# Kernel optimization log

Hardware: AMD Instinct MI355X
Metric: run time of the kernel (lower is better)

The kernel has to match this reference:

```python
import jax, jax.numpy as jnp
from jax import lax
import numpy as np

N_TOOLS = 50
DIM = 512
N_TOKENS = 8192
PARAM_DIM = 256


def setup_inputs() -> dict:
    key = jax.random.key(0)
    ks = jax.random.split(key, 8)
    s = 1.0 / np.sqrt(DIM)
    x = jax.random.normal(ks[0], (N_TOKENS, DIM), dtype=jnp.float32)
    router_w = jax.random.uniform(ks[1], (N_TOOLS, DIM), jnp.float32, -s, s)
    router_b = jax.random.uniform(ks[2], (N_TOOLS,), jnp.float32, -s, s)
    expert_w = jax.random.uniform(ks[3], (N_TOOLS, DIM, DIM), jnp.float32, -s, s)
    expert_b = jax.random.uniform(ks[4], (N_TOOLS, DIM), jnp.float32, -s, s)
    param_w = jax.random.uniform(ks[5], (PARAM_DIM, DIM), jnp.float32, -s, s)
    param_b = jax.random.uniform(ks[6], (PARAM_DIM,), jnp.float32, -s, s)
    return {"x": x, "router_w": router_w, "router_b": router_b,
            "expert_w": expert_w, "expert_b": expert_b,
            "param_w": param_w, "param_b": param_b}


def _moe_adapt(x, tool_idx, expert_w, expert_b):
    # Top-1 dispatch: for each expert i, y_i = x @ W_i.T + b_i, written only
    # where tool_idx == i. Scan over the fixed 50 experts (mirrors the torch
    # masked per-expert Linear loop) with masked select instead of scatter.
    def step(acc, wb):
        i, W, b = wb
        y = x @ W.T + b  # [N, dim]
        mask = (tool_idx == i)[:, None]
        return jnp.where(mask, y, acc), None

    init = jnp.zeros_like(x)
    acc, _ = lax.scan(step, init, (jnp.arange(N_TOOLS), expert_w, expert_b))
    return acc


def reference(x, router_w, router_b, expert_w, expert_b, param_w, param_b):
    tool_logits = x @ router_w.T + router_b            # [N, 50]
    tool_probs = jax.nn.softmax(tool_logits, axis=-1)   # [N, 50]
    tool_idx = jnp.argmax(tool_probs, axis=-1)          # [N] int
    adapted = _moe_adapt(x, tool_idx, expert_w, expert_b)  # [N, dim]
    params = x @ param_w.T + param_b                    # [N, 256]
    return (tool_idx, tool_probs, adapted, params)
```

## Files before the change

### kernel.cpp

```cpp
#include <hip/hip_runtime.h>
#include <hip/hip_bf16.h>
#include <math.h>

#define N_TOKENS 8192
#define DIM      512
#define N_TOOLS  50
#define PARAM_DIM 256
#define N_ROWBLK (N_TOKENS / 64)
#define MAX_BATCHES 192
#define LDSS 72

typedef float  f32x4 __attribute__((ext_vector_type(4)));
typedef short  s16x8 __attribute__((ext_vector_type(8)));
typedef short  s16x4 __attribute__((ext_vector_type(4)));

#define WS_IDX     0
#define WS_HIST    8192
#define WS_PHIST   14592
#define WS_OFFSETS 20992
#define WS_COUNTS  21056
#define WS_ORDER   21120
#define WS_BE      29312
#define WS_BM0     29504
#define WS_NB      29696

__device__ inline float bf2f(short s) {
    return __uint_as_float(((unsigned)(unsigned short)s) << 16);
}

__device__ inline s16x4 pk4(float a, float b, float c, float d) {
    __hip_bfloat162 p0 = __float22bfloat162_rn(make_float2(a, b));
    __hip_bfloat162 p1 = __float22bfloat162_rn(make_float2(c, d));
    union { __hip_bfloat162 h; short2 s; } u0, u1;
    u0.h = p0; u1.h = p1;
    s16x4 r; r[0] = u0.s.x; r[1] = u0.s.y; r[2] = u1.s.x; r[3] = u1.s.y;
    return r;
}

__global__ __launch_bounds__(256) void head_mfma(const float* __restrict__ x,
                                                 const float* __restrict__ pw,
                                                 const float* __restrict__ pb,
                                                 const float* __restrict__ rw,
                                                 const float* __restrict__ rb,
                                                 float* __restrict__ out_params,
                                                 float* __restrict__ probs,
                                                 float* __restrict__ out_idx,
                                                 int* __restrict__ idx_i,
                                                 int* __restrict__ hist) {
    int r0 = blockIdx.y * 64;
    bool isl = (blockIdx.x == 4);
    int c0 = isl ? 0 : blockIdx.x * 64;

    __shared__ short As[64 * LDSS];
    __shared__ short Bs[64 * LDSS];
    __shared__ short Al[64 * LDSS];
    __shared__ short Bl[64 * LDSS];
    __shared__ int rowcol[64];

    int tid = threadIdx.x;
    int wv = tid >> 6;
    int lane = tid & 63;
    int fm = lane & 15;
    int q = lane >> 4;

    const float* Bsrc = isl ? rw : pw;

    f32x4 acc[4] = {{0.f, 0.f, 0.f, 0.f}, {0.f, 0.f, 0.f, 0.f},
                    {0.f, 0.f, 0.f, 0.f}, {0.f, 0.f, 0.f, 0.f}};

    for (int k0 = 0; k0 < DIM; k0 += 64) {
#pragma unroll
        for (int i = 0; i < 4; ++i) {
            int u = i * 256 + tid;
            int r = u >> 4, g = u & 15;
            float4 v = *(const float4*)&x[(size_t)(r0 + r) * DIM + k0 + g * 4];
            s16x4 h = pk4(v.x, v.y, v.z, v.w);
            *(s16x4*)&As[r * LDSS + g * 4] = h;
            if (isl) {
                s16x4 l = pk4(v.x - bf2f(h[0]), v.y - bf2f(h[1]),
                              v.z - bf2f(h[2]), v.w - bf2f(h[3]));
                *(s16x4*)&Al[r * LDSS + g * 4] = l;
            }
        }
#pragma unroll
        for (int i = 0; i < 4; ++i) {
            int u = i * 256 + tid;
            int c = u >> 4, g = u & 15;
            float4 v = {0.f, 0.f, 0.f, 0.f};
            if (!isl || c < N_TOOLS)
                v = *(const float4*)&Bsrc[(size_t)(c0 + c) * DIM + k0 + g * 4];
            s16x4 h = pk4(v.x, v.y, v.z, v.w);
            *(s16x4*)&Bs[c * LDSS + g * 4] = h;
            if (isl) {
                s16x4 l = pk4(v.x - bf2f(h[0]), v.y - bf2f(h[1]),
                              v.z - bf2f(h[2]), v.w - bf2f(h[3]));
                *(s16x4*)&Bl[c * LDSS + g * 4] = l;
            }
        }
        __syncthreads();

#pragma unroll
        for (int kk = 0; kk < 64; kk += 32) {
            int ao = (wv * 16 + fm) * LDSS + kk + q * 8;
            s16x8 a = *(const s16x8*)&As[ao];
            if (!isl) {
#pragma unroll
                for (int n = 0; n < 4; ++n) {
                    s16x8 b = *(const s16x8*)&Bs[(n * 16 + fm) * LDSS + kk + q * 8];
                    acc[n] = __builtin_amdgcn_mfma_f32_16x16x32_bf16(a, b, acc[n], 0, 0, 0);
                }
            } else {
                s16x8 al = *(const s16x8*)&Al[ao];
#pragma unroll
                for (int n = 0; n < 4; ++n) {
                    int bo = (n * 16 + fm) * LDSS + kk + q * 8;
                    s16x8 b  = *(const s16x8*)&Bs[bo];
                    s16x8 bl = *(const s16x8*)&Bl[bo];
                    acc[n] = __builtin_amdgcn_mfma_f32_16x16x32_bf16(a,  b,  acc[n], 0, 0, 0);
                    acc[n] = __builtin_amdgcn_mfma_f32_16x16x32_bf16(a,  bl, acc[n], 0, 0, 0);
                    acc[n] = __builtin_amdgcn_mfma_f32_16x16x32_bf16(al, b,  acc[n], 0, 0, 0);
                }
            }
        }
        __syncthreads();
    }

    if (!isl) {
        float bias[4];
#pragma unroll
        for (int n = 0; n < 4; ++n) bias[n] = pb[c0 + n * 16 + fm];
#pragma unroll
        for (int r = 0; r < 4; ++r) {
            int row = r0 + wv * 16 + q * 4 + r;
            float* op = out_params + (size_t)row * PARAM_DIM + c0;
#pragma unroll
            for (int n = 0; n < 4; ++n) op[n * 16 + fm] = acc[n][r] + bias[n];
        }
    } else {
        float rbv[4];
#pragma unroll
        for (int n = 0; n < 4; ++n) {
            int c = n * 16 + fm;
            rbv[n] = (c < N_TOOLS) ? rb[c] : 0.f;
        }
#pragma unroll
        for (int rr = 0; rr < 4; ++rr) {
            int row_l = wv * 16 + q * 4 + rr;
            int row = r0 + row_l;
            float v[4];
            float vmax = -INFINITY; int vcol = N_TOOLS;
#pragma unroll
            for (int n = 0; n < 4; ++n) {
                int c = n * 16 + fm;
                v[n] = acc[n][rr] + rbv[n];
                if (c < N_TOOLS && v[n] > vmax) { vmax = v[n]; vcol = c; }
            }
#pragma unroll
            for (int s = 1; s < 16; s <<= 1) {
                float om = __shfl_xor(vmax, s, 64);
                int   oc = __shfl_xor(vcol, s, 64);
                if (om > vmax || (om == vmax && oc < vcol)) { vmax = om; vcol = oc; }
            }
            float e[4]; float esum = 0.f;
#pragma unroll
            for (int n = 0; n < 4; ++n) {
                int c = n * 16 + fm;
                e[n] = (c < N_TOOLS) ? expf(v[n] - vmax) : 0.f;
                esum += e[n];
            }
#pragma unroll
            for (int s = 1; s < 16; s <<= 1) esum += __shfl_xor(esum, s, 64);
            float inv = 1.f / esum;
#pragma unroll
            for (int n = 0; n < 4; ++n) {
                int c = n * 16 + fm;
                if (c < N_TOOLS) probs[(size_t)row * N_TOOLS + c] = e[n] * inv;
            }
            if (fm == 0) {
                out_idx[row] = (float)vcol;
                idx_i[row] = vcol;
                rowcol[row_l] = vcol;
            }
        }
        __syncthreads();
        if (wv == 0) {
            int myc = rowcol[lane];
            int cnt = 0;
            for (int e2 = 0; e2 < N_TOOLS; ++e2) {
                unsigned long long m = __ballot(myc == e2);
                if (lane == e2) cnt = __popcll(m);
            }
            if (lane < N_TOOLS) hist[blockIdx.y * N_TOOLS + lane] = cnt;
        }
    }
}

__global__ void scan_kernel(const int* __restrict__ hist,
                            int* __restrict__ offsets,
                            int* __restrict__ counts,
                            int* __restrict__ phist,
                            int* __restrict__ batch_e,
                            int* __restrict__ batch_m0,
                            int* __restrict__ nb_out) {
    int lane = threadIdx.x;
    int acc_c = 0;
    if (lane < N_TOOLS) {
#pragma unroll 4
        for (int b = 0; b < N_ROWBLK; ++b) {
            int t = hist[b * N_TOOLS + lane];
            phist[b * N_TOOLS + lane] = acc_c;
            acc_c += t;
        }
    }
    int c = (lane < N_TOOLS) ? acc_c : 0;
    int pre = c;
#pragma unroll
    for (int s = 1; s < 64; s <<= 1) {
        int v = __shfl_up(pre, s, 64);
        if (lane >= s) pre += v;
    }
    int excl = pre - c;
    if (lane < N_TOOLS) { offsets[lane] = excl; counts[lane] = c; }

    int nb_i = (lane < N_TOOLS) ? (c + 63) >> 6 : 0;
    int pre2 = nb_i;
#pragma unroll
    for (int s = 1; s < 64; s <<= 1) {
        int v = __shfl_up(pre2, s, 64);
        if (lane >= s) pre2 += v;
    }
    int bstart = pre2 - nb_i;
    for (int b = 0; b < nb_i; ++b) {
        batch_e[bstart + b] = lane;
        batch_m0[bstart + b] = b * 64;
    }
    if (lane == 63) nb_out[0] = pre2;
}

__global__ void reorder_kernel(const int* __restrict__ idx_i,
                               const int* __restrict__ offsets,
                               const int* __restrict__ phist,
                               int* __restrict__ order) {
    int b = blockIdx.x;
    int lane = threadIdx.x;
    int t = b * 64 + lane;
    int e = idx_i[t];
    unsigned long long lt = (1ull << lane) - 1ull;
    int rank = 0;
    for (int ex = 0; ex < N_TOOLS; ++ex) {
        unsigned long long m = __ballot(e == ex);
        if (e == ex) rank = __popcll(m & lt);
    }
    order[offsets[e] + phist[b * N_TOOLS + e] + rank] = t;
}

__global__ __launch_bounds__(256) void adapted_mfma(const float* __restrict__ x,
                                                    const float* __restrict__ ew,
                                                    const float* __restrict__ eb,
                                                    const int* __restrict__ order,
                                                    const int* __restrict__ batch_e,
                                                    const int* __restrict__ batch_m0,
                                                    const int* __restrict__ nb_ptr,
                                                    const int* __restrict__ offsets,
                                                    const int* __restrict__ counts,
                                                    float* __restrict__ out) {
    int b = blockIdx.y;
    if (b >= nb_ptr[0]) return;
    int e = batch_e[b];
    int m0 = batch_m0[b];
    int c0 = blockIdx.x * 64;
    int start = offsets[e] + m0;
    int len = counts[e] - m0;
    if (len > 64) len = 64;

    __shared__ short As[64 * LDSS];
    __shared__ short Bs[64 * LDSS];
    __shared__ int toks[64];

    int tid = threadIdx.x;
    if (tid < 64) toks[tid] = (tid < len) ? order[start + tid] : -1;
    __syncthreads();

    int wv = tid >> 6;
    int lane = tid & 63;
    int fm = lane & 15;
    int q = lane >> 4;

    const float* We = ew + (size_t)e * DIM * DIM;

    f32x4 acc[4] = {{0.f, 0.f, 0.f, 0.f}, {0.f, 0.f, 0.f, 0.f},
                    {0.f, 0.f, 0.f, 0.f}, {0.f, 0.f, 0.f, 0.f}};

    for (int k0 = 0; k0 < DIM; k0 += 64) {
#pragma unroll
        for (int i = 0; i < 4; ++i) {
            int u = i * 256 + tid;
            int r = u >> 4, g = u & 15;
            int tok = toks[r];
            float4 v = {0.f, 0.f, 0.f, 0.f};
            if (tok >= 0) v = *(const float4*)&x[(size_t)tok * DIM + k0 + g * 4];
            *(s16x4*)&As[r * LDSS + g * 4] = pk4(v.x, v.y, v.z, v.w);
        }
#pragma unroll
        for (int i = 0; i < 4; ++i) {
            int u = i * 256 + tid;
            int c = u >> 4, g = u & 15;
            float4 v = *(const float4*)&We[(size_t)(c0 + c) * DIM + k0 + g * 4];
            *(s16x4*)&Bs[c * LDSS + g * 4] = pk4(v.x, v.y, v.z, v.w);
        }
        __syncthreads();

#pragma unroll
        for (int kk = 0; kk < 64; kk += 32) {
            s16x8 a = *(const s16x8*)&As[(wv * 16 + fm) * LDSS + kk + q * 8];
#pragma unroll
            for (int n = 0; n < 4; ++n) {
                s16x8 bf = *(const s16x8*)&Bs[(n * 16 + fm) * LDSS + kk + q * 8];
                acc[n] = __builtin_amdgcn_mfma_f32_16x16x32_bf16(a, bf, acc[n], 0, 0, 0);
            }
        }
        __syncthreads();
    }

    float bias[4];
#pragma unroll
    for (int n = 0; n < 4; ++n) bias[n] = eb[(size_t)e * DIM + c0 + n * 16 + fm];

#pragma unroll
    for (int r = 0; r < 4; ++r) {
        int row = wv * 16 + q * 4 + r;
        int tok = toks[row];
        if (tok < 0) continue;
        float* op = out + (size_t)tok * DIM + c0;
#pragma unroll
        for (int n = 0; n < 4; ++n) op[n * 16 + fm] = acc[n][r] + bias[n];
    }
}

extern "C" void kernel_launch(void* const* d_in, const int* in_sizes, int n_in,
                              void* d_out, int out_size, void* d_ws, size_t ws_size,
                              hipStream_t stream) {
    const float* x        = (const float*)d_in[0];
    const float* router_w = (const float*)d_in[1];
    const float* router_b = (const float*)d_in[2];
    const float* expert_w = (const float*)d_in[3];
    const float* expert_b = (const float*)d_in[4];
    const float* param_w  = (const float*)d_in[5];
    const float* param_b  = (const float*)d_in[6];

    float* out = (float*)d_out;
    float* out_idx     = out;
    float* out_probs   = out + N_TOKENS;
    float* out_adapted = out + N_TOKENS + N_TOKENS * N_TOOLS;
    float* out_params  = out_adapted + (size_t)N_TOKENS * DIM;

    int* ws = (int*)d_ws;
    int* ws_idx     = ws + WS_IDX;
    int* ws_hist    = ws + WS_HIST;
    int* ws_phist   = ws + WS_PHIST;
    int* ws_offsets = ws + WS_OFFSETS;
    int* ws_counts  = ws + WS_COUNTS;
    int* ws_order   = ws + WS_ORDER;
    int* ws_be      = ws + WS_BE;
    int* ws_bm0     = ws + WS_BM0;
    int* ws_nb      = ws + WS_NB;

    head_mfma<<<dim3(5, N_ROWBLK), 256, 0, stream>>>(x, param_w, param_b,
                                                     router_w, router_b,
                                                     out_params, out_probs,
                                                     out_idx, ws_idx, ws_hist);

    scan_kernel<<<1, 64, 0, stream>>>(ws_hist, ws_offsets, ws_counts, ws_phist,
                                      ws_be, ws_bm0, ws_nb);

    reorder_kernel<<<N_ROWBLK, 64, 0, stream>>>(ws_idx, ws_offsets, ws_phist, ws_order);

    adapted_mfma<<<dim3(8, MAX_BATCHES), 256, 0, stream>>>(x, expert_w, expert_b,
                                                           ws_order, ws_be, ws_bm0, ws_nb,
                                                           ws_offsets, ws_counts, out_adapted);
}
```

Baseline: 176.7 us.

## Pre-convert x to bf16 hi/lo, register-prefetch tiles, parallelize histogram scan

Adds a kernel that converts x once into bf16 high and low-residual arrays in workspace, so the head and expert GEMMs load half-width data and no longer repeat the conversion per tile. Both GEMM kernels now prefetch the next K-tile into registers while the current tile is computed, overlapping global loads with MFMA work. The single-wave serial per-block scan is split into a per-expert parallel scan over 50 blocks plus a small offsets kernel. In exchange it adds two kernel launches and extra global traffic to write and reread the converted x.

Result: faster. 155.8 us (-11.8%).

```diff
diff --git a/kernel.cpp b/kernel.cpp
--- a/kernel.cpp
+++ b/kernel.cpp
@@ -23,6 +23,8 @@
 #define WS_BE      29312
 #define WS_BM0     29504
 #define WS_NB      29696
+#define WS_XH      32768
+#define WS_XL      2130944
 
 __device__ inline float bf2f(short s) {
     return __uint_as_float(((unsigned)(unsigned short)s) << 16);
@@ -37,7 +39,20 @@
     return r;
 }
 
-__global__ __launch_bounds__(256) void head_mfma(const float* __restrict__ x,
+__global__ __launch_bounds__(256) void cvt_x_kernel(const float* __restrict__ x,
+                                                    short* __restrict__ xh,
+                                                    short* __restrict__ xl) {
+    size_t i = (size_t)(blockIdx.x * 256 + threadIdx.x) * 4;
+    float4 v = *(const float4*)&x[i];
+    s16x4 h = pk4(v.x, v.y, v.z, v.w);
+    s16x4 l = pk4(v.x - bf2f(h[0]), v.y - bf2f(h[1]),
+                  v.z - bf2f(h[2]), v.w - bf2f(h[3]));
+    *(s16x4*)&xh[i] = h;
+    *(s16x4*)&xl[i] = l;
+}
+
+__global__ __launch_bounds__(256) void head_mfma(const short* __restrict__ xh,
+                                                 const short* __restrict__ xl,
                                                  const float* __restrict__ pw,
                                                  const float* __restrict__ pb,
                                                  const float* __restrict__ rw,
@@ -65,39 +80,71 @@
 
     const float* Bsrc = isl ? rw : pw;
 
+    int ar0 = tid >> 3, ag = tid & 7;
+    int ar1 = ar0 + 32;
+    const short* aptr0 = xh + (size_t)(r0 + ar0) * DIM + ag * 8;
+    const short* aptr1 = xh + (size_t)(r0 + ar1) * DIM + ag * 8;
+    const short* alptr0 = xl + (size_t)(r0 + ar0) * DIM + ag * 8;
+    const short* alptr1 = xl + (size_t)(r0 + ar1) * DIM + ag * 8;
+    int bc[4], bg[4];
+    const float* bptr[4];
+#pragma unroll
+    for (int i = 0; i < 4; ++i) {
+        int u = i * 256 + tid;
+        bc[i] = u >> 4; bg[i] = u & 15;
+        bptr[i] = Bsrc + (size_t)(c0 + bc[i]) * DIM + bg[i] * 4;
+    }
+
     f32x4 acc[4] = {{0.f, 0.f, 0.f, 0.f}, {0.f, 0.f, 0.f, 0.f},
                     {0.f, 0.f, 0.f, 0.f}, {0.f, 0.f, 0.f, 0.f}};
 
+    s16x8 apre0, apre1, alpre0, alpre1;
+    float4 bpre[4];
+    apre0 = *(const s16x8*)aptr0;
+    apre1 = *(const s16x8*)aptr1;
+    if (isl) { alpre0 = *(const s16x8*)alptr0; alpre1 = *(const s16x8*)alptr1; }
+#pragma unroll
+    for (int i = 0; i < 4; ++i) {
+        float4 v = {0.f, 0.f, 0.f, 0.f};
+        if (!isl || bc[i] < N_TOOLS) v = *(const float4*)bptr[i];
+        bpre[i] = v;
+    }
+
     for (int k0 = 0; k0 < DIM; k0 += 64) {
+        *(s16x8*)&As[ar0 * LDSS + ag * 8] = apre0;
+        *(s16x8*)&As[ar1 * LDSS + ag * 8] = apre1;
+        if (isl) {
+            *(s16x8*)&Al[ar0 * LDSS + ag * 8] = alpre0;
+            *(s16x8*)&Al[ar1 * LDSS + ag * 8] = alpre1;
+        }
 #pragma unroll
         for (int i = 0; i < 4; ++i) {
-            int u = i * 256 + tid;
-            int r = u >> 4, g = u & 15;
-            float4 v = *(const float4*)&x[(size_t)(r0 + r) * DIM + k0 + g * 4];
+            float4 v = bpre[i];
             s16x4 h = pk4(v.x, v.y, v.z, v.w);
-            *(s16x4*)&As[r * LDSS + g * 4] = h;
+            *(s16x4*)&Bs[bc[i] * LDSS + bg[i] * 4] = h;
             if (isl) {
                 s16x4 l = pk4(v.x - bf2f(h[0]), v.y - bf2f(h[1]),
                               v.z - bf2f(h[2]), v.w - bf2f(h[3]));
-                *(s16x4*)&Al[r * LDSS + g * 4] = l;
-            }
-        }
-#pragma unroll
-        for (int i = 0; i < 4; ++i) {
-            int u = i * 256 + tid;
-            int c = u >> 4, g = u & 15;
-            float4 v = {0.f, 0.f, 0.f, 0.f};
-            if (!isl || c < N_TOOLS)
-                v = *(const float4*)&Bsrc[(size_t)(c0 + c) * DIM + k0 + g * 4];
-            s16x4 h = pk4(v.x, v.y, v.z, v.w);
-            *(s16x4*)&Bs[c * LDSS + g * 4] = h;
+                *(s16x4*)&Bl[bc[i] * LDSS + bg[i] * 4] = l;
+            }
+        }
+        __syncthreads();
+
+        int kn = k0 + 64;
+        if (kn < DIM) {
+            apre0 = *(const s16x8*)(aptr0 + kn);
+            apre1 = *(const s16x8*)(aptr1 + kn);
             if (isl) {
-                s16x4 l = pk4(v.x - bf2f(h[0]), v.y - bf2f(h[1]),
-                              v.z - bf2f(h[2]), v.w - bf2f(h[3]));
-                *(s16x4*)&Bl[c * LDSS + g * 4] = l;
-            }
-        }
-        __syncthreads();
+                alpre0 = *(const s16x8*)(alptr0 + kn);
+                alpre1 = *(const s16x8*)(alptr1 + kn);
+            }
+#pragma unroll
+            for (int i = 0; i < 4; ++i) {
+                float4 v = {0.f, 0.f, 0.f, 0.f};
+                if (!isl || bc[i] < N_TOOLS) v = *(const float4*)(bptr[i] + kn);
+                bpre[i] = v;
+            }
+        }
 
 #pragma unroll
         for (int kk = 0; kk < 64; kk += 32) {
@@ -195,32 +242,46 @@
     }
 }
 
-__global__ void scan_kernel(const int* __restrict__ hist,
-                            int* __restrict__ offsets,
-                            int* __restrict__ counts,
-                            int* __restrict__ phist,
-                            int* __restrict__ batch_e,
-                            int* __restrict__ batch_m0,
-                            int* __restrict__ nb_out) {
+__global__ void scan1_kernel(const int* __restrict__ hist,
+                             int* __restrict__ phist,
+                             int* __restrict__ counts) {
+    int e = blockIdx.x;
+    int l = threadIdx.x;
+    int v0 = hist[l * N_TOOLS + e];
+    int v1 = hist[(64 + l) * N_TOOLS + e];
+    int s0 = v0;
+#pragma unroll
+    for (int s = 1; s < 64; s <<= 1) {
+        int t = __shfl_up(s0, s, 64);
+        if (l >= s) s0 += t;
+    }
+    int tot0 = __shfl(s0, 63, 64);
+    int s1 = v1;
+#pragma unroll
+    for (int s = 1; s < 64; s <<= 1) {
+        int t = __shfl_up(s1, s, 64);
+        if (l >= s) s1 += t;
+    }
+    s1 += tot0;
+    phist[l * N_TOOLS + e] = s0 - v0;
+    phist[(64 + l) * N_TOOLS + e] = s1 - v1;
+    if (l == 63) counts[e] = s1;
+}
+
+__global__ void scan2_kernel(const int* __restrict__ counts,
+                             int* __restrict__ offsets,
+                             int* __restrict__ batch_e,
+                             int* __restrict__ batch_m0,
+                             int* __restrict__ nb_out) {
     int lane = threadIdx.x;
-    int acc_c = 0;
-    if (lane < N_TOOLS) {
-#pragma unroll 4
-        for (int b = 0; b < N_ROWBLK; ++b) {
-            int t = hist[b * N_TOOLS + lane];
-            phist[b * N_TOOLS + lane] = acc_c;
-            acc_c += t;
-        }
-    }
-    int c = (lane < N_TOOLS) ? acc_c : 0;
+    int c = (lane < N_TOOLS) ? counts[lane] : 0;
     int pre = c;
 #pragma unroll
     for (int s = 1; s < 64; s <<= 1) {
         int v = __shfl_up(pre, s, 64);
         if (lane >= s) pre += v;
     }
-    int excl = pre - c;
-    if (lane < N_TOOLS) { offsets[lane] = excl; counts[lane] = c; }
+    if (lane < N_TOOLS) offsets[lane] = pre - c;
 
     int nb_i = (lane < N_TOOLS) ? (c + 63) >> 6 : 0;
     int pre2 = nb_i;
@@ -254,7 +315,7 @@
     order[offsets[e] + phist[b * N_TOOLS + e] + rank] = t;
 }
 
-__global__ __launch_bounds__(256) void adapted_mfma(const float* __restrict__ x,
+__global__ __launch_bounds__(256) void adapted_mfma(const short* __restrict__ xh,
                                                     const float* __restrict__ ew,
                                                     const float* __restrict__ eb,
                                                     const int* __restrict__ order,
@@ -288,27 +349,47 @@
 
     const float* We = ew + (size_t)e * DIM * DIM;
 
+    int ar0 = tid >> 3, ag = tid & 7;
+    int ar1 = ar0 + 32;
+    int tok0 = toks[ar0], tok1 = toks[ar1];
+    const short* aptr0 = (tok0 >= 0) ? xh + (size_t)tok0 * DIM + ag * 8 : nullptr;
+    const short* aptr1 = (tok1 >= 0) ? xh + (size_t)tok1 * DIM + ag * 8 : nullptr;
+    int bc[4], bg[4];
+    const float* bptr[4];
+#pragma unroll
+    for (int i = 0; i < 4; ++i) {
+        int u = i * 256 + tid;
+        bc[i] = u >> 4; bg[i] = u & 15;
+        bptr[i] = We + (size_t)(c0 + bc[i]) * DIM + bg[i] * 4;
+    }
+
     f32x4 acc[4] = {{0.f, 0.f, 0.f, 0.f}, {0.f, 0.f, 0.f, 0.f},
                     {0.f, 0.f, 0.f, 0.f}, {0.f, 0.f, 0.f, 0.f}};
 
+    const s16x8 z8 = {0, 0, 0, 0, 0, 0, 0, 0};
+    s16x8 apre0 = aptr0 ? *(const s16x8*)aptr0 : z8;
+    s16x8 apre1 = aptr1 ? *(const s16x8*)aptr1 : z8;
+    float4 bpre[4];
+#pragma unroll
+    for (int i = 0; i < 4; ++i) bpre[i] = *(const float4*)bptr[i];
+
     for (int k0 = 0; k0 < DIM; k0 += 64) {
+        *(s16x8*)&As[ar0 * LDSS + ag * 8] = apre0;
+        *(s16x8*)&As[ar1 * LDSS + ag * 8] = apre1;
 #pragma unroll
         for (int i = 0; i < 4; ++i) {
-            int u = i * 256 + tid;
-            int r = u >> 4, g = u & 15;
-            int tok = toks[r];
-            float4 v = {0.f, 0.f, 0.f, 0.f};
-            if (tok >= 0) v = *(const float4*)&x[(size_t)tok * DIM + k0 + g * 4];
-            *(s16x4*)&As[r * LDSS + g * 4] = pk4(v.x, v.y, v.z, v.w);
-        }
-#pragma unroll
-        for (int i = 0; i < 4; ++i) {
-            int u = i * 256 + tid;
-            int c = u >> 4, g = u & 15;
-            float4 v = *(const float4*)&We[(size_t)(c0 + c) * DIM + k0 + g * 4];
-            *(s16x4*)&Bs[c * LDSS + g * 4] = pk4(v.x, v.y, v.z, v.w);
+            float4 v = bpre[i];
+            *(s16x4*)&Bs[bc[i] * LDSS + bg[i] * 4] = pk4(v.x, v.y, v.z, v.w);
         }
         __syncthreads();
+
+        int kn = k0 + 64;
+        if (kn < DIM) {
+            apre0 = aptr0 ? *(const s16x8*)(aptr0 + kn) : z8;
+            apre1 = aptr1 ? *(const s16x8*)(aptr1 + kn) : z8;
+#pragma unroll
+            for (int i = 0; i < 4; ++i) bpre[i] = *(const float4*)(bptr[i] + kn);
+        }
 
 #pragma unroll
         for (int kk = 0; kk < 64; kk += 32) {
@@ -364,18 +445,23 @@
     int* ws_be      = ws + WS_BE;
     int* ws_bm0     = ws + WS_BM0;
     int* ws_nb      = ws + WS_NB;
-
-    head_mfma<<<dim3(5, N_ROWBLK), 256, 0, stream>>>(x, param_w, param_b,
+    short* ws_xh    = (short*)(ws + WS_XH);
+    short* ws_xl    = (short*)(ws + WS_XL);
+
+    cvt_x_kernel<<<N_TOKENS * DIM / 4 / 256, 256, 0, stream>>>(x, ws_xh, ws_xl);
+
+    head_mfma<<<dim3(5, N_ROWBLK), 256, 0, stream>>>(ws_xh, ws_xl, param_w, param_b,
                                                      router_w, router_b,
                                                      out_params, out_probs,
                                                      out_idx, ws_idx, ws_hist);
 
-    scan_kernel<<<1, 64, 0, stream>>>(ws_hist, ws_offsets, ws_counts, ws_phist,
-                                      ws_be, ws_bm0, ws_nb);
+    scan1_kernel<<<N_TOOLS, 64, 0, stream>>>(ws_hist, ws_phist, ws_counts);
+
+    scan2_kernel<<<1, 64, 0, stream>>>(ws_counts, ws_offsets, ws_be, ws_bm0, ws_nb);
 
     reorder_kernel<<<N_ROWBLK, 64, 0, stream>>>(ws_idx, ws_offsets, ws_phist, ws_order);
 
-    adapted_mfma<<<dim3(8, MAX_BATCHES), 256, 0, stream>>>(x, expert_w, expert_b,
+    adapted_mfma<<<dim3(8, MAX_BATCHES), 256, 0, stream>>>(ws_xh, expert_w, expert_b,
                                                            ws_order, ws_be, ws_bm0, ws_nb,
                                                            ws_offsets, ws_counts, out_adapted);
 }
```

## Cache bf16 x, keep full expert weight tile in LDS, merge scan and reorder

Applied to the files above, without the earlier changes.

The router block now writes a bf16 copy of x to workspace. The expert GEMM reads that copy instead of re-gathering fp32 x and converting it. Each expert block loads the whole 64-column weight slice (all K) into LDS once and loops over every 64-token batch of its expert, so weights are fetched once per expert column tile rather than once per batch. The separate scan and reorder kernels are merged into a single 1024-thread kernel, and A operands are streamed from global memory into registers with prefetch. The cost is a larger LDS footprint (about 72KB per block, lower occupancy) and load imbalance, since one block serially handles every token routed to its expert.

Result: slower. 188.0 us (+6.4%).

```diff
diff --git a/kernel.cpp b/kernel.cpp
--- a/kernel.cpp
+++ b/kernel.cpp
@@ -7,8 +7,8 @@
 #define N_TOOLS  50
 #define PARAM_DIM 256
 #define N_ROWBLK (N_TOKENS / 64)
-#define MAX_BATCHES 192
 #define LDSS 72
+#define BSREG (64 * LDSS)
 
 typedef float  f32x4 __attribute__((ext_vector_type(4)));
 typedef short  s16x8 __attribute__((ext_vector_type(8)));
@@ -16,13 +16,10 @@
 
 #define WS_IDX     0
 #define WS_HIST    8192
-#define WS_PHIST   14592
-#define WS_OFFSETS 20992
-#define WS_COUNTS  21056
-#define WS_ORDER   21120
-#define WS_BE      29312
-#define WS_BM0     29504
-#define WS_NB      29696
+#define WS_COUNTS  14592
+#define WS_OFFSETS 14656
+#define WS_ORDER   14720
+#define WS_XH      32768
 
 __device__ inline float bf2f(short s) {
     return __uint_as_float(((unsigned)(unsigned short)s) << 16);
@@ -34,6 +31,13 @@
     union { __hip_bfloat162 h; short2 s; } u0, u1;
     u0.h = p0; u1.h = p1;
     s16x4 r; r[0] = u0.s.x; r[1] = u0.s.y; r[2] = u1.s.x; r[3] = u1.s.y;
+    return r;
+}
+
+__device__ inline s16x8 cat8(s16x4 a, s16x4 b) {
+    s16x8 r;
+    r[0] = a[0]; r[1] = a[1]; r[2] = a[2]; r[3] = a[3];
+    r[4] = b[0]; r[5] = b[1]; r[6] = b[2]; r[7] = b[3];
     return r;
 }
 
@@ -46,15 +50,13 @@
                                                  float* __restrict__ probs,
                                                  float* __restrict__ out_idx,
                                                  int* __restrict__ idx_i,
-                                                 int* __restrict__ hist) {
+                                                 int* __restrict__ hist,
+                                                 short* __restrict__ xh) {
     int r0 = blockIdx.y * 64;
     bool isl = (blockIdx.x == 4);
-    int c0 = isl ? 0 : blockIdx.x * 64;
-
-    __shared__ short As[64 * LDSS];
-    __shared__ short Bs[64 * LDSS];
-    __shared__ short Al[64 * LDSS];
-    __shared__ short Bl[64 * LDSS];
+    int c0 = blockIdx.x * 64;
+
+    __shared__ short Bs[8 * BSREG];
     __shared__ int rowcol[64];
 
     int tid = threadIdx.x;
@@ -63,80 +65,139 @@
     int fm = lane & 15;
     int q = lane >> 4;
 
-    const float* Bsrc = isl ? rw : pw;
+    int row = r0 + wv * 16 + fm;
+    const float* ax = x + (size_t)row * DIM + q * 8;
 
     f32x4 acc[4] = {{0.f, 0.f, 0.f, 0.f}, {0.f, 0.f, 0.f, 0.f},
                     {0.f, 0.f, 0.f, 0.f}, {0.f, 0.f, 0.f, 0.f}};
 
-    for (int k0 = 0; k0 < DIM; k0 += 64) {
+    if (!isl) {
+#pragma unroll
+        for (int i = 0; i < 32; ++i) {
+            int u = i * 256 + tid;
+            int col = u >> 7, g = u & 127;
+            float4 v = *(const float4*)&pw[(size_t)(c0 + col) * DIM + g * 4];
+            int kt = g >> 4, kw = (g & 15) * 4;
+            *(s16x4*)&Bs[kt * BSREG + col * LDSS + kw] = pk4(v.x, v.y, v.z, v.w);
+        }
+        __syncthreads();
+
+        float4 f0 = *(const float4*)(ax);
+        float4 f1 = *(const float4*)(ax + 4);
+        float4 f2 = *(const float4*)(ax + 32);
+        float4 f3 = *(const float4*)(ax + 36);
+
+        for (int kt = 0; kt < 8; ++kt) {
+            float4 n0, n1, n2, n3;
+            if (kt < 7) {
+                const float* axn = ax + (kt + 1) * 64;
+                n0 = *(const float4*)(axn);
+                n1 = *(const float4*)(axn + 4);
+                n2 = *(const float4*)(axn + 32);
+                n3 = *(const float4*)(axn + 36);
+            }
+            s16x8 a0 = cat8(pk4(f0.x, f0.y, f0.z, f0.w), pk4(f1.x, f1.y, f1.z, f1.w));
+            s16x8 a1 = cat8(pk4(f2.x, f2.y, f2.z, f2.w), pk4(f3.x, f3.y, f3.z, f3.w));
+#pragma unroll
+            for (int kk = 0; kk < 64; kk += 32) {
+                s16x8 a = kk ? a1 : a0;
+#pragma unroll
+                for (int n = 0; n < 4; ++n) {
+                    s16x8 b = *(const s16x8*)&Bs[kt * BSREG + (n * 16 + fm) * LDSS + kk + q * 8];
+                    acc[n] = __builtin_amdgcn_mfma_f32_16x16x32_bf16(a, b, acc[n], 0, 0, 0);
+                }
+            }
+            f0 = n0; f1 = n1; f2 = n2; f3 = n3;
+        }
+
+        float bias[4];
+#pragma unroll
+        for (int n = 0; n < 4; ++n) bias[n] = pb[c0 + n * 16 + fm];
+#pragma unroll
+        for (int r = 0; r < 4; ++r) {
+            int orow = r0 + wv * 16 + q * 4 + r;
+            float* op = out_params + (size_t)orow * PARAM_DIM + c0;
+#pragma unroll
+            for (int n = 0; n < 4; ++n) op[n * 16 + fm] = acc[n][r] + bias[n];
+        }
+    } else {
+        short* BsL = Bs;
+        short* BlL = Bs + BSREG;
+        int col[4], g[4];
+        const float* bptr[4];
 #pragma unroll
         for (int i = 0; i < 4; ++i) {
             int u = i * 256 + tid;
-            int r = u >> 4, g = u & 15;
-            float4 v = *(const float4*)&x[(size_t)(r0 + r) * DIM + k0 + g * 4];
-            s16x4 h = pk4(v.x, v.y, v.z, v.w);
-            *(s16x4*)&As[r * LDSS + g * 4] = h;
-            if (isl) {
+            col[i] = u >> 4; g[i] = u & 15;
+            bptr[i] = rw + (size_t)col[i] * DIM + g[i] * 4;
+        }
+        float4 bpre[4];
+#pragma unroll
+        for (int i = 0; i < 4; ++i) {
+            float4 v = {0.f, 0.f, 0.f, 0.f};
+            if (col[i] < N_TOOLS) v = *(const float4*)bptr[i];
+            bpre[i] = v;
+        }
+        float4 f0 = *(const float4*)(ax);
+        float4 f1 = *(const float4*)(ax + 4);
+        float4 f2 = *(const float4*)(ax + 32);
+        float4 f3 = *(const float4*)(ax + 36);
+
+        for (int kt = 0; kt < 8; ++kt) {
+#pragma unroll
+            for (int i = 0; i < 4; ++i) {
+                float4 v = bpre[i];
+                s16x4 h = pk4(v.x, v.y, v.z, v.w);
+                *(s16x4*)&BsL[col[i] * LDSS + g[i] * 4] = h;
                 s16x4 l = pk4(v.x - bf2f(h[0]), v.y - bf2f(h[1]),
                               v.z - bf2f(h[2]), v.w - bf2f(h[3]));
-                *(s16x4*)&Al[r * LDSS + g * 4] = l;
-            }
-        }
-#pragma unroll
-        for (int i = 0; i < 4; ++i) {
-            int u = i * 256 + tid;
-            int c = u >> 4, g = u & 15;
-            float4 v = {0.f, 0.f, 0.f, 0.f};
-            if (!isl || c < N_TOOLS)
-                v = *(const float4*)&Bsrc[(size_t)(c0 + c) * DIM + k0 + g * 4];
-            s16x4 h = pk4(v.x, v.y, v.z, v.w);
-            *(s16x4*)&Bs[c * LDSS + g * 4] = h;
-            if (isl) {
-                s16x4 l = pk4(v.x - bf2f(h[0]), v.y - bf2f(h[1]),
-                              v.z - bf2f(h[2]), v.w - bf2f(h[3]));
-                *(s16x4*)&Bl[c * LDSS + g * 4] = l;
-            }
-        }
-        __syncthreads();
-
-#pragma unroll
-        for (int kk = 0; kk < 64; kk += 32) {
-            int ao = (wv * 16 + fm) * LDSS + kk + q * 8;
-            s16x8 a = *(const s16x8*)&As[ao];
-            if (!isl) {
-#pragma unroll
-                for (int n = 0; n < 4; ++n) {
-                    s16x8 b = *(const s16x8*)&Bs[(n * 16 + fm) * LDSS + kk + q * 8];
-                    acc[n] = __builtin_amdgcn_mfma_f32_16x16x32_bf16(a, b, acc[n], 0, 0, 0);
+                *(s16x4*)&BlL[col[i] * LDSS + g[i] * 4] = l;
+            }
+            __syncthreads();
+
+            s16x4 h0 = pk4(f0.x, f0.y, f0.z, f0.w);
+            s16x4 h1 = pk4(f1.x, f1.y, f1.z, f1.w);
+            s16x4 h2 = pk4(f2.x, f2.y, f2.z, f2.w);
+            s16x4 h3 = pk4(f3.x, f3.y, f3.z, f3.w);
+            s16x8 a0h = cat8(h0, h1), a1h = cat8(h2, h3);
+            s16x8 a0l = cat8(pk4(f0.x - bf2f(h0[0]), f0.y - bf2f(h0[1]), f0.z - bf2f(h0[2]), f0.w - bf2f(h0[3])),
+                             pk4(f1.x - bf2f(h1[0]), f1.y - bf2f(h1[1]), f1.z - bf2f(h1[2]), f1.w - bf2f(h1[3])));
+            s16x8 a1l = cat8(pk4(f2.x - bf2f(h2[0]), f2.y - bf2f(h2[1]), f2.z - bf2f(h2[2]), f2.w - bf2f(h2[3])),
+                             pk4(f3.x - bf2f(h3[0]), f3.y - bf2f(h3[1]), f3.z - bf2f(h3[2]), f3.w - bf2f(h3[3])));
+            *(s16x8*)&xh[(size_t)row * DIM + kt * 64 + q * 8] = a0h;
+            *(s16x8*)&xh[(size_t)row * DIM + kt * 64 + 32 + q * 8] = a1h;
+
+            if (kt < 7) {
+                const float* axn = ax + (kt + 1) * 64;
+                f0 = *(const float4*)(axn);
+                f1 = *(const float4*)(axn + 4);
+                f2 = *(const float4*)(axn + 32);
+                f3 = *(const float4*)(axn + 36);
+#pragma unroll
+                for (int i = 0; i < 4; ++i) {
+                    float4 v = {0.f, 0.f, 0.f, 0.f};
+                    if (col[i] < N_TOOLS) v = *(const float4*)(bptr[i] + (kt + 1) * 64);
+                    bpre[i] = v;
                 }
-            } else {
-                s16x8 al = *(const s16x8*)&Al[ao];
+            }
+
+#pragma unroll
+            for (int kk = 0; kk < 64; kk += 32) {
+                s16x8 ah = kk ? a1h : a0h;
+                s16x8 al = kk ? a1l : a0l;
 #pragma unroll
                 for (int n = 0; n < 4; ++n) {
                     int bo = (n * 16 + fm) * LDSS + kk + q * 8;
-                    s16x8 b  = *(const s16x8*)&Bs[bo];
-                    s16x8 bl = *(const s16x8*)&Bl[bo];
-                    acc[n] = __builtin_amdgcn_mfma_f32_16x16x32_bf16(a,  b,  acc[n], 0, 0, 0);
-                    acc[n] = __builtin_amdgcn_mfma_f32_16x16x32_bf16(a,  bl, acc[n], 0, 0, 0);
+                    s16x8 b  = *(const s16x8*)&BsL[bo];
+                    s16x8 bl = *(const s16x8*)&BlL[bo];
+                    acc[n] = __builtin_amdgcn_mfma_f32_16x16x32_bf16(ah, b,  acc[n], 0, 0, 0);
+                    acc[n] = __builtin_amdgcn_mfma_f32_16x16x32_bf16(ah, bl, acc[n], 0, 0, 0);
                     acc[n] = __builtin_amdgcn_mfma_f32_16x16x32_bf16(al, b,  acc[n], 0, 0, 0);
                 }
             }
-        }
-        __syncthreads();
-    }
-
-    if (!isl) {
-        float bias[4];
-#pragma unroll
-        for (int n = 0; n < 4; ++n) bias[n] = pb[c0 + n * 16 + fm];
-#pragma unroll
-        for (int r = 0; r < 4; ++r) {
-            int row = r0 + wv * 16 + q * 4 + r;
-            float* op = out_params + (size_t)row * PARAM_DIM + c0;
-#pragma unroll
-            for (int n = 0; n < 4; ++n) op[n * 16 + fm] = acc[n][r] + bias[n];
-        }
-    } else {
+            __syncthreads();
+        }
+
         float rbv[4];
 #pragma unroll
         for (int n = 0; n < 4; ++n) {
@@ -146,7 +207,7 @@
 #pragma unroll
         for (int rr = 0; rr < 4; ++rr) {
             int row_l = wv * 16 + q * 4 + rr;
-            int row = r0 + row_l;
+            int orow = r0 + row_l;
             float v[4];
             float vmax = -INFINITY; int vcol = N_TOOLS;
 #pragma unroll
@@ -174,11 +235,11 @@
 #pragma unroll
             for (int n = 0; n < 4; ++n) {
                 int c = n * 16 + fm;
-                if (c < N_TOOLS) probs[(size_t)row * N_TOOLS + c] = e[n] * inv;
+                if (c < N_TOOLS) probs[(size_t)orow * N_TOOLS + c] = e[n] * inv;
             }
             if (fm == 0) {
-                out_idx[row] = (float)vcol;
-                idx_i[row] = vcol;
+                out_idx[orow] = (float)vcol;
+                idx_i[orow] = vcol;
                 rowcol[row_l] = vcol;
             }
         }
@@ -195,145 +256,139 @@
     }
 }
 
-__global__ void scan_kernel(const int* __restrict__ hist,
-                            int* __restrict__ offsets,
-                            int* __restrict__ counts,
-                            int* __restrict__ phist,
-                            int* __restrict__ batch_e,
-                            int* __restrict__ batch_m0,
-                            int* __restrict__ nb_out) {
-    int lane = threadIdx.x;
-    int acc_c = 0;
-    if (lane < N_TOOLS) {
-#pragma unroll 4
-        for (int b = 0; b < N_ROWBLK; ++b) {
-            int t = hist[b * N_TOOLS + lane];
-            phist[b * N_TOOLS + lane] = acc_c;
-            acc_c += t;
-        }
-    }
-    int c = (lane < N_TOOLS) ? acc_c : 0;
-    int pre = c;
-#pragma unroll
-    for (int s = 1; s < 64; s <<= 1) {
-        int v = __shfl_up(pre, s, 64);
-        if (lane >= s) pre += v;
-    }
-    int excl = pre - c;
-    if (lane < N_TOOLS) { offsets[lane] = excl; counts[lane] = c; }
-
-    int nb_i = (lane < N_TOOLS) ? (c + 63) >> 6 : 0;
-    int pre2 = nb_i;
-#pragma unroll
-    for (int s = 1; s < 64; s <<= 1) {
-        int v = __shfl_up(pre2, s, 64);
-        if (lane >= s) pre2 += v;
-    }
-    int bstart = pre2 - nb_i;
-    for (int b = 0; b < nb_i; ++b) {
-        batch_e[bstart + b] = lane;
-        batch_m0[bstart + b] = b * 64;
-    }
-    if (lane == 63) nb_out[0] = pre2;
-}
-
-__global__ void reorder_kernel(const int* __restrict__ idx_i,
-                               const int* __restrict__ offsets,
-                               const int* __restrict__ phist,
-                               int* __restrict__ order) {
-    int b = blockIdx.x;
-    int lane = threadIdx.x;
-    int t = b * 64 + lane;
-    int e = idx_i[t];
-    unsigned long long lt = (1ull << lane) - 1ull;
-    int rank = 0;
-    for (int ex = 0; ex < N_TOOLS; ++ex) {
-        unsigned long long m = __ballot(e == ex);
-        if (e == ex) rank = __popcll(m & lt);
-    }
-    order[offsets[e] + phist[b * N_TOOLS + e] + rank] = t;
-}
-
-__global__ __launch_bounds__(256) void adapted_mfma(const float* __restrict__ x,
+__global__ __launch_bounds__(1024) void scan_reorder(const int* __restrict__ hist,
+                                                     const int* __restrict__ idx_i,
+                                                     int* __restrict__ counts,
+                                                     int* __restrict__ offsets,
+                                                     int* __restrict__ order) {
+    __shared__ int phist[N_ROWBLK * N_TOOLS];
+    __shared__ int cnt_s[64];
+    __shared__ int off_s[64];
+    int l = threadIdx.x & 63;
+    int w = threadIdx.x >> 6;
+
+    for (int e = w; e < N_TOOLS; e += 16) {
+        int v0 = hist[l * N_TOOLS + e];
+        int v1 = hist[(64 + l) * N_TOOLS + e];
+        int s0 = v0;
+#pragma unroll
+        for (int s = 1; s < 64; s <<= 1) {
+            int t = __shfl_up(s0, s, 64);
+            if (l >= s) s0 += t;
+        }
+        int tot0 = __shfl(s0, 63, 64);
+        int s1 = v1;
+#pragma unroll
+        for (int s = 1; s < 64; s <<= 1) {
+            int t = __shfl_up(s1, s, 64);
+            if (l >= s) s1 += t;
+        }
+        s1 += tot0;
+        phist[l * N_TOOLS + e] = s0 - v0;
+        phist[(64 + l) * N_TOOLS + e] = s1 - v1;
+        if (l == 63) cnt_s[e] = s1;
+    }
+    __syncthreads();
+
+    if (w == 0) {
+        int c = (l < N_TOOLS) ? cnt_s[l] : 0;
+        int pre = c;
+#pragma unroll
+        for (int s = 1; s < 64; s <<= 1) {
+            int v = __shfl_up(pre, s, 64);
+            if (l >= s) pre += v;
+        }
+        off_s[l] = pre - c;
+        if (l < N_TOOLS) { offsets[l] = pre - c; counts[l] = c; }
+    }
+    __syncthreads();
+
+    unsigned long long lt = (1ull << l) - 1ull;
+    for (int bb = w; bb < N_ROWBLK; bb += 16) {
+        int t = bb * 64 + l;
+        int e = idx_i[t];
+        int rank = 0;
+        for (int ex = 0; ex < N_TOOLS; ++ex) {
+            unsigned long long m = __ballot(e == ex);
+            if (e == ex) rank = __popcll(m & lt);
+        }
+        order[off_s[e] + phist[bb * N_TOOLS + e] + rank] = t;
+    }
+}
+
+__global__ __launch_bounds__(256) void adapted_mfma(const short* __restrict__ xh,
                                                     const float* __restrict__ ew,
                                                     const float* __restrict__ eb,
                                                     const int* __restrict__ order,
-                                                    const int* __restrict__ batch_e,
-                                                    const int* __restrict__ batch_m0,
-                                                    const int* __restrict__ nb_ptr,
                                                     const int* __restrict__ offsets,
                                                     const int* __restrict__ counts,
                                                     float* __restrict__ out) {
-    int b = blockIdx.y;
-    if (b >= nb_ptr[0]) return;
-    int e = batch_e[b];
-    int m0 = batch_m0[b];
+    int e = blockIdx.y;
+    int cnt = counts[e];
+    if (cnt == 0) return;
     int c0 = blockIdx.x * 64;
-    int start = offsets[e] + m0;
-    int len = counts[e] - m0;
-    if (len > 64) len = 64;
-
-    __shared__ short As[64 * LDSS];
-    __shared__ short Bs[64 * LDSS];
-    __shared__ int toks[64];
+    int start = offsets[e];
+
+    __shared__ short Bs[8 * BSREG];
 
     int tid = threadIdx.x;
-    if (tid < 64) toks[tid] = (tid < len) ? order[start + tid] : -1;
-    __syncthreads();
-
     int wv = tid >> 6;
     int lane = tid & 63;
     int fm = lane & 15;
     int q = lane >> 4;
 
     const float* We = ew + (size_t)e * DIM * DIM;
-
-    f32x4 acc[4] = {{0.f, 0.f, 0.f, 0.f}, {0.f, 0.f, 0.f, 0.f},
-                    {0.f, 0.f, 0.f, 0.f}, {0.f, 0.f, 0.f, 0.f}};
-
-    for (int k0 = 0; k0 < DIM; k0 += 64) {
-#pragma unroll
-        for (int i = 0; i < 4; ++i) {
-            int u = i * 256 + tid;
-            int r = u >> 4, g = u & 15;
-            int tok = toks[r];
-            float4 v = {0.f, 0.f, 0.f, 0.f};
-            if (tok >= 0) v = *(const float4*)&x[(size_t)tok * DIM + k0 + g * 4];
-            *(s16x4*)&As[r * LDSS + g * 4] = pk4(v.x, v.y, v.z, v.w);
-        }
-#pragma unroll
-        for (int i = 0; i < 4; ++i) {
-            int u = i * 256 + tid;
-            int c = u >> 4, g = u & 15;
-            float4 v = *(const float4*)&We[(size_t)(c0 + c) * DIM + k0 + g * 4];
-            *(s16x4*)&Bs[c * LDSS + g * 4] = pk4(v.x, v.y, v.z, v.w);
-        }
-        __syncthreads();
-
-#pragma unroll
-        for (int kk = 0; kk < 64; kk += 32) {
-            s16x8 a = *(const s16x8*)&As[(wv * 16 + fm) * LDSS + kk + q * 8];
-#pragma unroll
-            for (int n = 0; n < 4; ++n) {
-                s16x8 bf = *(const s16x8*)&Bs[(n * 16 + fm) * LDSS + kk + q * 8];
-                acc[n] = __builtin_amdgcn_mfma_f32_16x16x32_bf16(a, bf, acc[n], 0, 0, 0);
-            }
-        }
-        __syncthreads();
-    }
+#pragma unroll
+    for (int i = 0; i < 32; ++i) {
+        int u = i * 256 + tid;
+        int col = u >> 7, g = u & 127;
+        float4 v = *(const float4*)&We[(size_t)(c0 + col) * DIM + g * 4];
+        int kt = g >> 4, kw = (g & 15) * 4;
+        *(s16x4*)&Bs[kt * BSREG + col * LDSS + kw] = pk4(v.x, v.y, v.z, v.w);
+    }
+    __syncthreads();
 
     float bias[4];
 #pragma unroll
     for (int n = 0; n < 4; ++n) bias[n] = eb[(size_t)e * DIM + c0 + n * 16 + fm];
 
-#pragma unroll
-    for (int r = 0; r < 4; ++r) {
-        int row = wv * 16 + q * 4 + r;
-        int tok = toks[row];
-        if (tok < 0) continue;
-        float* op = out + (size_t)tok * DIM + c0;
-#pragma unroll
-        for (int n = 0; n < 4; ++n) op[n * 16 + fm] = acc[n][r] + bias[n];
+    for (int m0 = 0; m0 < cnt; m0 += 64) {
+        int idxA = m0 + wv * 16 + fm;
+        int tokA = (idxA < cnt) ? order[start + idxA] : 0;
+        const short* aph = xh + (size_t)tokA * DIM + q * 8;
+
+        f32x4 acc[4] = {{0.f, 0.f, 0.f, 0.f}, {0.f, 0.f, 0.f, 0.f},
+                        {0.f, 0.f, 0.f, 0.f}, {0.f, 0.f, 0.f, 0.f}};
+
+        s16x8 a0 = *(const s16x8*)(aph);
+        s16x8 a1 = *(const s16x8*)(aph + 32);
+        for (int kt = 0; kt < 8; ++kt) {
+            s16x8 a0n, a1n;
+            if (kt < 7) {
+                a0n = *(const s16x8*)(aph + (kt + 1) * 64);
+                a1n = *(const s16x8*)(aph + (kt + 1) * 64 + 32);
+            }
+#pragma unroll
+            for (int kk = 0; kk < 64; kk += 32) {
+                s16x8 a = kk ? a1 : a0;
+#pragma unroll
+                for (int n = 0; n < 4; ++n) {
+                    s16x8 b = *(const s16x8*)&Bs[kt * BSREG + (n * 16 + fm) * LDSS + kk + q * 8];
+                    acc[n] = __builtin_amdgcn_mfma_f32_16x16x32_bf16(a, b, acc[n], 0, 0, 0);
+                }
+            }
+            a0 = a0n; a1 = a1n;
+        }
+
+#pragma unroll
+        for (int r = 0; r < 4; ++r) {
+            int idxE = m0 + wv * 16 + q * 4 + r;
+            if (idxE >= cnt) continue;
+            int tokE = order[start + idxE];
+            float* op = out + (size_t)tokE * DIM + c0;
+#pragma unroll
+            for (int n = 0; n < 4; ++n) op[n * 16 + fm] = acc[n][r] + bias[n];
+        }
     }
 }
 
@@ -357,25 +412,19 @@
     int* ws = (int*)d_ws;
     int* ws_idx     = ws + WS_IDX;
     int* ws_hist    = ws + WS_HIST;
-    int* ws_phist   = ws + WS_PHIST;
+    int* ws_counts  = ws + WS_COUNTS;
     int* ws_offsets = ws + WS_OFFSETS;
-    int* ws_counts  = ws + WS_COUNTS;
     int* ws_order   = ws + WS_ORDER;
-    int* ws_be      = ws + WS_BE;
-    int* ws_bm0     = ws + WS_BM0;
-    int* ws_nb      = ws + WS_NB;
+    short* ws_xh    = (short*)(ws + WS_XH);
 
     head_mfma<<<dim3(5, N_ROWBLK), 256, 0, stream>>>(x, param_w, param_b,
                                                      router_w, router_b,
                                                      out_params, out_probs,
-                                                     out_idx, ws_idx, ws_hist);
-
-    scan_kernel<<<1, 64, 0, stream>>>(ws_hist, ws_offsets, ws_counts, ws_phist,
-                                      ws_be, ws_bm0, ws_nb);
-
-    reorder_kernel<<<N_ROWBLK, 64, 0, stream>>>(ws_idx, ws_offsets, ws_phist, ws_order);
-
-    adapted_mfma<<<dim3(8, MAX_BATCHES), 256, 0, stream>>>(x, expert_w, expert_b,
-                                                           ws_order, ws_be, ws_bm0, ws_nb,
-                                                           ws_offsets, ws_counts, out_adapted);
-}
+                                                     out_idx, ws_idx, ws_hist, ws_xh);
+
+    scan_reorder<<<1, 1024, 0, stream>>>(ws_hist, ws_idx, ws_counts, ws_offsets, ws_order);
+
+    adapted_mfma<<<dim3(8, N_TOOLS), 256, 0, stream>>>(ws_xh, expert_w, expert_b,
+                                                       ws_order, ws_offsets, ws_counts,
+                                                       out_adapted);
+}
```
